# Optimization experiments

Hardware: AMD Instinct MI355X
Metric: run time of the kernel (lower is better)

## Reference

```python
import jax, jax.numpy as jnp
import numpy as np

B, C, Hf, Wf, HM, P = 64, 2048, 16, 16, 256, 10  # P = num_parts, NP = graph nodes
NP = P - 1
EPS = 1e-5  # BatchNorm eps

def bn_eval(x, g, b, rm, rv):
    return (x - rm) * jax.lax.rsqrt(rv + EPS) * g + b

def setup_inputs() -> dict:
    key = jax.random.key(0)
    ks = jax.random.split(key, 6)
    return {
        "x_global": jax.random.normal(ks[0], (B, C, Hf, Wf), jnp.float32),
        "x_gcn": jax.random.normal(ks[1], (B, C, Hf, Wf), jnp.float32),
        "mask": jax.random.randint(ks[2], (B, 1, HM, HM), 0, P, jnp.int32),
        "adj": jax.random.uniform(ks[3], (B, NP, NP), jnp.float32),
        "W1": jax.random.normal(ks[4], (C, C), jnp.float32) * 0.02,
        "b1": jnp.zeros((C,), jnp.float32),
        "g1": jnp.ones((NP * C,), jnp.float32), "be1": jnp.zeros((NP * C,), jnp.float32),
        "rm1": jnp.zeros((NP * C,), jnp.float32), "rv1": jnp.ones((NP * C,), jnp.float32),
        "W2": jax.random.normal(ks[5], (C, C), jnp.float32) * 0.02,
        "b2": jnp.zeros((C,), jnp.float32),
        "g2": jnp.ones((NP * C,), jnp.float32), "be2": jnp.zeros((NP * C,), jnp.float32),
        "rm2": jnp.zeros((NP * C,), jnp.float32), "rv2": jnp.ones((NP * C,), jnp.float32),
        "gb_g": jnp.ones((C,), jnp.float32), "gb_b": jnp.zeros((C,), jnp.float32),
        "gb_rm": jnp.zeros((C,), jnp.float32), "gb_rv": jnp.ones((C,), jnp.float32),
        "gn_g": jnp.ones((C,), jnp.float32), "gn_b": jnp.zeros((C,), jnp.float32),
        "gn_rm": jnp.zeros((C,), jnp.float32), "gn_rv": jnp.ones((C,), jnp.float32),
    }

def gc_layer(x, adj, Wt, bias, g, be, rm, rv):
    # GraphConvolution: matmul -> bmm(adj) -> bias -> BN over flattened (B, NP*C)
    s = jnp.einsum('bpc,cd->bpd', x, Wt)
    o = jnp.einsum('bpq,bqd->bpd', adj, s) + bias
    flat = o.reshape(o.shape[0], -1)
    return bn_eval(flat, g, be, rm, rv).reshape(o.shape)

def reference(x_global, x_gcn, mask, adj, W1, b1, g1, be1, rm1, rv1,
              W2, b2, g2, be2, rm2, rv2, gb_g, gb_b, gb_rm, gb_rv,
              gn_g, gn_b, gn_rm, gn_rv):
    # --- global branch: GAP + bottleneck BN (eval) ---
    feat_global = x_global.mean(axis=(2, 3))                      # (B, C)
    bnfeat_global = bn_eval(feat_global, gb_g, gb_b, gb_rm, gb_rv)

    # --- nearest-neighbor downsample of mask to feature-map size ---
    stride = HM // Hf
    mr = mask[:, 0, ::stride, ::stride]                           # (B, h, w)

    # one-hot part masks for classes 1..P-1: (B, h, w, NP)
    onehot = (mr[..., None] == jnp.arange(1, P)).astype(jnp.float32)
    counts = onehot.sum(axis=(1, 2))                              # (B, NP)

    # deterministic part dropout: drop the first present part per image
    drop = jnp.argmax(counts > 0, axis=1) + 1                     # (B,)
    keep = (mr != drop[:, None, None]).astype(jnp.float32)        # (B, h, w)
    x_self = x_gcn * keep[:, None, :, :]

    # segment mean pooling per part: (B, NP, C)
    denom = (counts + 1e-8)[..., None]
    mask_feat = jnp.einsum('bchw,bhwp->bpc', x_gcn, onehot) / denom
    self_feat = jnp.einsum('bchw,bhwp->bpc', x_self, onehot) / denom

    def gcn(x):
        x1 = jax.nn.relu(gc_layer(x, adj, W1, b1, g1, be1, rm1, rv1))
        x2 = jax.nn.relu(gc_layer(x1, adj, W2, b2, g2, be2, rm2, rv2))
        return x2.mean(axis=1), x2.reshape(x2.shape[0], -1)

    feat_gcn, feat_gcn_cat = gcn(mask_feat)
    feat_self, feat_self_cat = gcn(self_feat)
    bnfeat_gcn = bn_eval(feat_gcn, gn_g, gn_b, gn_rm, gn_rv)
    bnfeat_self = bn_eval(feat_self, gn_g, gn_b, gn_rm, gn_rv)

    # concatenate eval-mode outputs into one array: (B, 3*C + 2*NP*C)
    return jnp.concatenate([bnfeat_global, bnfeat_gcn, bnfeat_self,
                            feat_gcn_cat, feat_self_cat], axis=1)
```

## Files before the change

### kernel.cpp

```cpp
#include <hip/hip_runtime.h>
#include <cstdint>
#include <cstddef>

#define EPSV 1e-5f

typedef __bf16 bf16x8 __attribute__((ext_vector_type(8)));
typedef float f32x4 __attribute__((ext_vector_type(4)));

__device__ __forceinline__ unsigned short f2bf(float f) {
  unsigned int u = __float_as_uint(f);
  u += 0x7FFFu + ((u >> 16) & 1u);
  return (unsigned short)(u >> 16);
}

__device__ __forceinline__ void async_copy16(const void* src, void* dst_lds) {
  __builtin_amdgcn_global_load_lds(
      (const __attribute__((address_space(1))) void*)src,
      (__attribute__((address_space(3))) void*)dst_lds, 16, 0, 0);
}

__global__ __launch_bounds__(256) void prep(
    const float* __restrict__ W1, const float* __restrict__ W2,
    unsigned short* __restrict__ Wt1, unsigned short* __restrict__ Wt2,
    const float* __restrict__ xg, const float* __restrict__ gb_g,
    const float* __restrict__ gb_b, const float* __restrict__ gb_rm,
    const float* __restrict__ gb_rv, float* __restrict__ out,
    const int* __restrict__ mask, int* __restrict__ partid,
    float* __restrict__ invden, int* __restrict__ dropm1) {
  int blk = blockIdx.x;
  if (blk < 8192) {
    int z = blk >> 12;
    int rem = blk & 4095;
    int by = rem >> 6, bx = rem & 63;
    const float* W = z ? W2 : W1;
    unsigned short* Wt = z ? Wt2 : Wt1;
    __shared__ float tile[32][33];
    int tx = threadIdx.x & 31;
    int ty = threadIdx.x >> 5;
    int k0 = by * 32, n0 = bx * 32;
#pragma unroll
    for (int i = 0; i < 32; i += 8)
      tile[ty + i][tx] = W[(size_t)(k0 + ty + i) * 2048 + n0 + tx];
    __syncthreads();
#pragma unroll
    for (int i = 0; i < 32; i += 8)
      Wt[(size_t)(n0 + ty + i) * 2048 + k0 + tx] = f2bf(tile[tx][ty + i]);
  } else if (blk < 40960) {
    int gw = (blk - 8192) * 4 + (threadIdx.x >> 6);
    int lane = threadIdx.x & 63;
    float4 v = ((const float4*)(xg + (size_t)gw * 256))[lane];
    float s = v.x + v.y + v.z + v.w;
#pragma unroll
    for (int o = 32; o > 0; o >>= 1) s += __shfl_xor(s, o, 64);
    if (lane == 0) {
      int b = gw >> 11, c = gw & 2047;
      float m = s * (1.f / 256.f);
      out[(size_t)b * 43008 + c] =
          (m - gb_rm[c]) / sqrtf(gb_rv[c] + EPSV) * gb_g[c] + gb_b[c];
    }
  } else {
    int b = blk - 40960;
    int t = threadIdx.x;
    int h = t >> 4, w = t & 15;
    int m = mask[(size_t)b * 65536 + h * 4096 + w * 16];
    partid[b * 256 + t] = m;
    __shared__ int cnt[10];
    if (t < 10) cnt[t] = 0;
    __syncthreads();
    atomicAdd(&cnt[m], 1);
    __syncthreads();
    if (t == 0) {
      int dp = 0;
      for (int p = 8; p >= 0; p--)
        if (cnt[p + 1] > 0) dp = p;
      dropm1[b] = dp;
    }
    if (t < 9) invden[b * 9 + t] = 1.f / ((float)cnt[t + 1] + 1e-8f);
  }
}

__global__ __launch_bounds__(256) void kpool_mfma(
    const float* __restrict__ x, const int* __restrict__ partid,
    const float* __restrict__ invden, const int* __restrict__ dropm1,
    unsigned short* __restrict__ Abuf) {
  __shared__ unsigned short As[64 * 264];
  __shared__ unsigned short Bs[16 * 264];
  __shared__ int pid[256];
  const int t = threadIdx.x;
  const int b = blockIdx.y;
  const int c0 = blockIdx.x * 64;

  pid[t] = partid[b * 256 + t];

  const float4* xgp = (const float4*)(x + ((size_t)(b * 2048 + c0)) * 256);
#pragma unroll
  for (int it = 0; it < 16; it++) {
    int idx = t + it * 256;
    float4 v = xgp[idx];
    int row = idx >> 6, sc = (idx & 63) * 4;
    ushort4 h;
    h.x = f2bf(v.x); h.y = f2bf(v.y); h.z = f2bf(v.z); h.w = f2bf(v.w);
    *(ushort4*)&As[row * 264 + sc] = h;
  }
  __syncthreads();
  {
    int p = t >> 4, s0 = (t & 15) * 16;
#pragma unroll
    for (int j = 0; j < 16; j++)
      Bs[p * 264 + s0 + j] =
          (pid[s0 + j] == p + 1) ? (unsigned short)0x3F80 : (unsigned short)0;
  }
  __syncthreads();

  const int wave = t >> 6;
  const int l16 = t & 15;
  const int quad = (t & 63) >> 4;
  f32x4 acc = (f32x4){0.f, 0.f, 0.f, 0.f};
#pragma unroll
  for (int ks = 0; ks < 8; ks++) {
    bf16x8 a = *(const bf16x8*)&As[(wave * 16 + l16) * 264 + ks * 32 + quad * 8];
    bf16x8 bf = *(const bf16x8*)&Bs[l16 * 264 + ks * 32 + quad * 8];
    acc = __builtin_amdgcn_mfma_f32_16x16x32_bf16(a, bf, acc, 0, 0, 0);
  }

  if (l16 < 9) {
    int p = l16;
    float inv = invden[b * 9 + p];
    int dm1 = dropm1[b];
    int cbase = c0 + wave * 16 + quad * 4;
    ushort4 hm;
    hm.x = f2bf(acc[0] * inv);
    hm.y = f2bf(acc[1] * inv);
    hm.z = f2bf(acc[2] * inv);
    hm.w = f2bf(acc[3] * inv);
    ushort4 hs = (p == dm1) ? (ushort4){0, 0, 0, 0} : hm;
    *(ushort4*)&Abuf[(size_t)(b * 9 + p) * 2048 + cbase] = hm;
    *(ushort4*)&Abuf[(size_t)((64 + b) * 9 + p) * 2048 + cbase] = hs;
  }
}

#define GK 2048
#define SPART (1152 * 2048)
__global__ __launch_bounds__(256) void gemm_db(
    const unsigned short* __restrict__ A, const unsigned short* __restrict__ Bt,
    float* __restrict__ S) {
  __shared__ unsigned short As[2][128 * 64];
  __shared__ unsigned short Bs[2][128 * 64];
  const int tid = threadIdx.x;
  const int lane = tid & 63;
  const int wave = tid >> 6;
  const int wm = (wave >> 1) << 6;
  const int wn = (wave & 1) << 6;
  const int quad = lane >> 4;
  const int l16 = lane & 15;
  const int by = blockIdx.y;
  const int bx = blockIdx.x;
  const int kz = blockIdx.z;

  const unsigned short* Ag = A + (size_t)by * 128 * GK;
  const unsigned short* Bg = Bt + (size_t)bx * 128 * GK;
  S += (size_t)kz * SPART;

  f32x4 acc[4][4];
#pragma unroll
  for (int i = 0; i < 4; i++)
#pragma unroll
    for (int j = 0; j < 4; j++) acc[i][j] = (f32x4){0.f, 0.f, 0.f, 0.f};

  int srow[4], scol[4];
#pragma unroll
  for (int s = 0; s < 4; s++) {
    int idx = tid + s * 256;
    srow[s] = idx >> 3;
    scol[s] = ((idx & 7) ^ (srow[s] & 7)) * 8;
  }

  const int kbeg = kz * 512;

#define STAGE(buf, kk)                                                        \
  do {                                                                        \
    _Pragma("unroll") for (int s = 0; s < 4; s++) {                           \
      int idx = tid + s * 256;                                                \
      async_copy16(Ag + (size_t)srow[s] * GK + (kk) + scol[s],                \
                   &As[buf][idx * 8]);                                        \
    }                                                                         \
    _Pragma("unroll") for (int s = 0; s < 4; s++) {                           \
      int idx = tid + s * 256;                                                \
      async_copy16(Bg + (size_t)srow[s] * GK + (kk) + scol[s],                \
                   &Bs[buf][idx * 8]);                                        \
    }                                                                         \
  } while (0)

  STAGE(0, kbeg);
  asm volatile("s_waitcnt vmcnt(0)" ::: "memory");
  __syncthreads();

  for (int it = 0; it < 8; it++) {
    const int cur = it & 1;
    if (it < 7) STAGE(cur ^ 1, kbeg + (it + 1) * 64);

#pragma unroll
    for (int ks = 0; ks < 2; ks++) {
      bf16x8 af[4], bfr[4];
#pragma unroll
      for (int i = 0; i < 4; i++) {
        int row = wm + i * 16 + l16;
        int slot = row * 8 + ((ks * 4 + quad) ^ (row & 7));
        af[i] = *(const bf16x8*)&As[cur][slot * 8];
      }
#pragma unroll
      for (int j = 0; j < 4; j++) {
        int row = wn + j * 16 + l16;
        int slot = row * 8 + ((ks * 4 + quad) ^ (row & 7));
        bfr[j] = *(const bf16x8*)&Bs[cur][slot * 8];
      }
#pragma unroll
      for (int i = 0; i < 4; i++)
#pragma unroll
        for (int j = 0; j < 4; j++)
          acc[i][j] = __builtin_amdgcn_mfma_f32_16x16x32_bf16(
              af[i], bfr[j], acc[i][j], 0, 0, 0);
    }

    if (it < 7) {
      asm volatile("s_waitcnt vmcnt(0)" ::: "memory");
      __syncthreads();
    }
  }

#pragma unroll
  for (int i = 0; i < 4; i++)
#pragma unroll
    for (int j = 0; j < 4; j++)
#pragma unroll
      for (int r = 0; r < 4; r++) {
        int m = by * 128 + wm + i * 16 + quad * 4 + r;
        int n = bx * 128 + wn + j * 16 + l16;
        S[(size_t)m * 2048 + n] = acc[i][j][r];
      }
}

__global__ __launch_bounds__(256) void epi_mid(
    const float* __restrict__ S, const float* __restrict__ adj,
    const float* __restrict__ bias, const float* __restrict__ g,
    const float* __restrict__ be, const float* __restrict__ rm,
    const float* __restrict__ rv, unsigned short* __restrict__ Aout) {
  int idx = blockIdx.x * 256 + threadIdx.x;
  int d = idx & 2047;
  int bb = idx >> 11;
  int b = bb & 63;
  float s[9];
#pragma unroll
  for (int q = 0; q < 9; q++) {
    size_t off = (size_t)(bb * 9 + q) * 2048 + d;
    s[q] = S[off] + S[off + SPART] + S[off + 2 * SPART] + S[off + 3 * SPART];
  }
#pragma unroll
  for (int p = 0; p < 9; p++) {
    float o = bias[d];
#pragma unroll
    for (int q = 0; q < 9; q++) o += adj[b * 81 + p * 9 + q] * s[q];
    int f = p * 2048 + d;
    float v = (o - rm[f]) / sqrtf(rv[f] + EPSV) * g[f] + be[f];
    v = fmaxf(v, 0.f);
    Aout[(size_t)(bb * 9 + p) * 2048 + d] = f2bf(v);
  }
}

__global__ __launch_bounds__(256) void epi_final(
    const float* __restrict__ S, const float* __restrict__ adj,
    const float* __restrict__ bias, const float* __restrict__ g,
    const float* __restrict__ be, const float* __restrict__ rm,
    const float* __restrict__ rv, const float* __restrict__ gn_g,
    const float* __restrict__ gn_b, const float* __restrict__ gn_rm,
    const float* __restrict__ gn_rv, float* __restrict__ out) {
  int idx = blockIdx.x * 256 + threadIdx.x;
  int d = idx & 2047;
  int bb = idx >> 11;
  int b = bb & 63;
  bool selfb = bb >= 64;
  float s[9];
#pragma unroll
  for (int q = 0; q < 9; q++) {
    size_t off = (size_t)(bb * 9 + q) * 2048 + d;
    s[q] = S[off] + S[off + SPART] + S[off + 2 * SPART] + S[off + 3 * SPART];
  }
  float* orow = out + (size_t)b * 43008;
  size_t catbase = selfb ? 24576 : 6144;
  float mean = 0.f;
#pragma unroll
  for (int p = 0; p < 9; p++) {
    float o = bias[d];
#pragma unroll
    for (int q = 0; q < 9; q++) o += adj[b * 81 + p * 9 + q] * s[q];
    int f = p * 2048 + d;
    float v = (o - rm[f]) / sqrtf(rv[f] + EPSV) * g[f] + be[f];
    v = fmaxf(v, 0.f);
    mean += v;
    orow[catbase + f] = v;
  }
  mean *= (1.f / 9.f);
  orow[(selfb ? 4096 : 2048) + d] =
      (mean - gn_rm[d]) / sqrtf(gn_rv[d] + EPSV) * gn_g[d] + gn_b[d];
}

extern "C" void kernel_launch(void* const* d_in, const int* in_sizes, int n_in,
                              void* d_out, int out_size, void* d_ws,
                              size_t ws_size, hipStream_t stream) {
  const float* x_global = (const float*)d_in[0];
  const float* x_gcn = (const float*)d_in[1];
  const int* mask = (const int*)d_in[2];
  const float* adj = (const float*)d_in[3];
  const float* W1 = (const float*)d_in[4];
  const float* b1 = (const float*)d_in[5];
  const float* g1 = (const float*)d_in[6];
  const float* be1 = (const float*)d_in[7];
  const float* rm1 = (const float*)d_in[8];
  const float* rv1 = (const float*)d_in[9];
  const float* W2 = (const float*)d_in[10];
  const float* b2 = (const float*)d_in[11];
  const float* g2 = (const float*)d_in[12];
  const float* be2 = (const float*)d_in[13];
  const float* rm2 = (const float*)d_in[14];
  const float* rv2 = (const float*)d_in[15];
  const float* gb_g = (const float*)d_in[16];
  const float* gb_b = (const float*)d_in[17];
  const float* gb_rm = (const float*)d_in[18];
  const float* gb_rv = (const float*)d_in[19];
  const float* gn_g = (const float*)d_in[20];
  const float* gn_b = (const float*)d_in[21];
  const float* gn_rm = (const float*)d_in[22];
  const float* gn_rv = (const float*)d_in[23];
  float* out = (float*)d_out;

  char* ws = (char*)d_ws;
  int* partid = (int*)(ws);
  float* invden = (float*)(ws + 65536);
  int* dropm1 = (int*)(ws + 67840);
  unsigned short* Abuf = (unsigned short*)(ws + 131072);
  unsigned short* Wt1 = (unsigned short*)(ws + 4849664);
  unsigned short* Wt2 = (unsigned short*)(ws + 13238272);
  float* S = (float*)(ws + 21626880);

  prep<<<41024, 256, 0, stream>>>(W1, W2, Wt1, Wt2, x_global, gb_g, gb_b,
                                  gb_rm, gb_rv, out, mask, partid, invden,
                                  dropm1);
  kpool_mfma<<<dim3(32, 64), 256, 0, stream>>>(x_gcn, partid, invden, dropm1,
                                               Abuf);
  gemm_db<<<dim3(16, 9, 4), 256, 0, stream>>>(Abuf, Wt1, S);
  epi_mid<<<1024, 256, 0, stream>>>(S, adj, b1, g1, be1, rm1, rv1, Abuf);
  gemm_db<<<dim3(16, 9, 4), 256, 0, stream>>>(Abuf, Wt2, S);
  epi_final<<<1024, 256, 0, stream>>>(S, adj, b2, g2, be2, rm2, rv2, gn_g,
                                      gn_b, gn_rm, gn_rv, out);
}
```

Baseline: 411.1 us.

## Apply adjacency before the weight GEMM and fuse BN epilogue into GEMM

Uses associativity, adj·(X·W) = (adj·X)·W, so the 9x9 adjacency mix is applied to the pooled features in kpool (with the dropped part handled by subtracting its contribution) and to the layer-1 activations in a small kadj2 kernel. This lets the GEMM epilogue apply bias, BatchNorm and ReLU directly. The split-K partial-sum buffer S and its fp32 write and reduction traffic are removed. The GEMM now runs the full K loop per block over 144 blocks instead of 576, which lowers parallelism on a large GPU. The adj-mixed intermediate is rounded to bf16 before the GEMM, and the final mean is computed by re-reading the output.

```diff
diff --git a/kernel.cpp b/kernel.cpp
--- a/kernel.cpp
+++ b/kernel.cpp
@@ -11,6 +11,10 @@
   unsigned int u = __float_as_uint(f);
   u += 0x7FFFu + ((u >> 16) & 1u);
   return (unsigned short)(u >> 16);
+}
+
+__device__ __forceinline__ float bf2f(unsigned short h) {
+  return __uint_as_float(((unsigned int)h) << 16);
 }
 
 __device__ __forceinline__ void async_copy16(const void* src, void* dst_lds) {
@@ -82,10 +86,11 @@
 __global__ __launch_bounds__(256) void kpool_mfma(
     const float* __restrict__ x, const int* __restrict__ partid,
     const float* __restrict__ invden, const int* __restrict__ dropm1,
-    unsigned short* __restrict__ Abuf) {
+    const float* __restrict__ adj, unsigned short* __restrict__ A1) {
   __shared__ unsigned short As[64 * 264];
   __shared__ unsigned short Bs[16 * 264];
   __shared__ int pid[256];
+  __shared__ float sbuf[4][4][16][4];
   const int t = threadIdx.x;
   const int b = blockIdx.y;
   const int c0 = blockIdx.x * 64;
@@ -123,27 +128,50 @@
     acc = __builtin_amdgcn_mfma_f32_16x16x32_bf16(a, bf, acc, 0, 0, 0);
   }
 
+  {
+    float inv = (l16 < 9) ? invden[b * 9 + l16] : 0.f;
+    sbuf[wave][quad][l16][0] = acc[0] * inv;
+    sbuf[wave][quad][l16][1] = acc[1] * inv;
+    sbuf[wave][quad][l16][2] = acc[2] * inv;
+    sbuf[wave][quad][l16][3] = acc[3] * inv;
+  }
+  __syncthreads();
+
   if (l16 < 9) {
     int p = l16;
-    float inv = invden[b * 9 + p];
     int dm1 = dropm1[b];
+    const float* ap = adj + b * 81 + p * 9;
+    float om[4] = {0.f, 0.f, 0.f, 0.f};
+#pragma unroll
+    for (int q = 0; q < 9; q++) {
+      float aq = ap[q];
+#pragma unroll
+      for (int r = 0; r < 4; r++) om[r] += aq * sbuf[wave][quad][q][r];
+    }
+    float ad = ap[dm1];
+    float os[4];
+#pragma unroll
+    for (int r = 0; r < 4; r++) os[r] = om[r] - ad * sbuf[wave][quad][dm1][r];
+
     int cbase = c0 + wave * 16 + quad * 4;
-    ushort4 hm;
-    hm.x = f2bf(acc[0] * inv);
-    hm.y = f2bf(acc[1] * inv);
-    hm.z = f2bf(acc[2] * inv);
-    hm.w = f2bf(acc[3] * inv);
-    ushort4 hs = (p == dm1) ? (ushort4){0, 0, 0, 0} : hm;
-    *(ushort4*)&Abuf[(size_t)(b * 9 + p) * 2048 + cbase] = hm;
-    *(ushort4*)&Abuf[(size_t)((64 + b) * 9 + p) * 2048 + cbase] = hs;
+    ushort4 hm, hs;
+    hm.x = f2bf(om[0]); hm.y = f2bf(om[1]);
+    hm.z = f2bf(om[2]); hm.w = f2bf(om[3]);
+    hs.x = f2bf(os[0]); hs.y = f2bf(os[1]);
+    hs.z = f2bf(os[2]); hs.w = f2bf(os[3]);
+    *(ushort4*)&A1[(size_t)(b * 9 + p) * 2048 + cbase] = hm;
+    *(ushort4*)&A1[(size_t)((64 + b) * 9 + p) * 2048 + cbase] = hs;
   }
 }
 
 #define GK 2048
-#define SPART (1152 * 2048)
-__global__ __launch_bounds__(256) void gemm_db(
+template <int LAYER>
+__global__ __launch_bounds__(256) void gemm_fused(
     const unsigned short* __restrict__ A, const unsigned short* __restrict__ Bt,
-    float* __restrict__ S) {
+    const float* __restrict__ bias, const float* __restrict__ g,
+    const float* __restrict__ be, const float* __restrict__ rm,
+    const float* __restrict__ rv, unsigned short* __restrict__ Aout,
+    float* __restrict__ out) {
   __shared__ unsigned short As[2][128 * 64];
   __shared__ unsigned short Bs[2][128 * 64];
   const int tid = threadIdx.x;
@@ -155,11 +183,9 @@
   const int l16 = lane & 15;
   const int by = blockIdx.y;
   const int bx = blockIdx.x;
-  const int kz = blockIdx.z;
 
   const unsigned short* Ag = A + (size_t)by * 128 * GK;
   const unsigned short* Bg = Bt + (size_t)bx * 128 * GK;
-  S += (size_t)kz * SPART;
 
   f32x4 acc[4][4];
 #pragma unroll
@@ -174,8 +200,6 @@
     srow[s] = idx >> 3;
     scol[s] = ((idx & 7) ^ (srow[s] & 7)) * 8;
   }
-
-  const int kbeg = kz * 512;
 
 #define STAGE(buf, kk)                                                        \
   do {                                                                        \
@@ -191,13 +215,13 @@
     }                                                                         \
   } while (0)
 
-  STAGE(0, kbeg);
+  STAGE(0, 0);
   asm volatile("s_waitcnt vmcnt(0)" ::: "memory");
   __syncthreads();
 
-  for (int it = 0; it < 8; it++) {
+  for (int it = 0; it < 32; it++) {
     const int cur = it & 1;
-    if (it < 7) STAGE(cur ^ 1, kbeg + (it + 1) * 64);
+    if (it < 31) STAGE(cur ^ 1, (it + 1) * 64);
 
 #pragma unroll
     for (int ks = 0; ks < 2; ks++) {
@@ -222,7 +246,7 @@
               af[i], bfr[j], acc[i][j], 0, 0, 0);
     }
 
-    if (it < 7) {
+    if (it < 31) {
       asm volatile("s_waitcnt vmcnt(0)" ::: "memory");
       __syncthreads();
     }
@@ -231,77 +255,64 @@
 #pragma unroll
   for (int i = 0; i < 4; i++)
 #pragma unroll
-    for (int j = 0; j < 4; j++)
-#pragma unroll
-      for (int r = 0; r < 4; r++) {
-        int m = by * 128 + wm + i * 16 + quad * 4 + r;
+    for (int r = 0; r < 4; r++) {
+      int m = by * 128 + wm + i * 16 + quad * 4 + r;
+      int grp = m / 9;
+      int p = m - grp * 9;
+#pragma unroll
+      for (int j = 0; j < 4; j++) {
         int n = bx * 128 + wn + j * 16 + l16;
-        S[(size_t)m * 2048 + n] = acc[i][j][r];
+        int f = p * 2048 + n;
+        float v = acc[i][j][r] + bias[n];
+        v = (v - rm[f]) / sqrtf(rv[f] + EPSV) * g[f] + be[f];
+        v = fmaxf(v, 0.f);
+        if (LAYER == 1) {
+          Aout[(size_t)m * 2048 + n] = f2bf(v);
+        } else {
+          int b = grp & 63;
+          size_t base = (size_t)b * 43008 + ((grp >> 6) ? 24576 : 6144);
+          out[base + f] = v;
+        }
       }
-}
-
-__global__ __launch_bounds__(256) void epi_mid(
-    const float* __restrict__ S, const float* __restrict__ adj,
-    const float* __restrict__ bias, const float* __restrict__ g,
-    const float* __restrict__ be, const float* __restrict__ rm,
-    const float* __restrict__ rv, unsigned short* __restrict__ Aout) {
-  int idx = blockIdx.x * 256 + threadIdx.x;
-  int d = idx & 2047;
-  int bb = idx >> 11;
+    }
+}
+
+__global__ __launch_bounds__(256) void kadj2(
+    const unsigned short* __restrict__ A2, const float* __restrict__ adj,
+    unsigned short* __restrict__ A2p) {
+  int t = blockIdx.x * 256 + threadIdx.x;
+  int d = t & 2047;
+  int bb = t >> 11;
   int b = bb & 63;
   float s[9];
 #pragma unroll
-  for (int q = 0; q < 9; q++) {
-    size_t off = (size_t)(bb * 9 + q) * 2048 + d;
-    s[q] = S[off] + S[off + SPART] + S[off + 2 * SPART] + S[off + 3 * SPART];
-  }
+  for (int q = 0; q < 9; q++) s[q] = bf2f(A2[(size_t)(bb * 9 + q) * 2048 + d]);
+  const float* ap = adj + b * 81;
 #pragma unroll
   for (int p = 0; p < 9; p++) {
-    float o = bias[d];
-#pragma unroll
-    for (int q = 0; q < 9; q++) o += adj[b * 81 + p * 9 + q] * s[q];
-    int f = p * 2048 + d;
-    float v = (o - rm[f]) / sqrtf(rv[f] + EPSV) * g[f] + be[f];
-    v = fmaxf(v, 0.f);
-    Aout[(size_t)(bb * 9 + p) * 2048 + d] = f2bf(v);
-  }
-}
-
-__global__ __launch_bounds__(256) void epi_final(
-    const float* __restrict__ S, const float* __restrict__ adj,
-    const float* __restrict__ bias, const float* __restrict__ g,
-    const float* __restrict__ be, const float* __restrict__ rm,
-    const float* __restrict__ rv, const float* __restrict__ gn_g,
-    const float* __restrict__ gn_b, const float* __restrict__ gn_rm,
-    const float* __restrict__ gn_rv, float* __restrict__ out) {
-  int idx = blockIdx.x * 256 + threadIdx.x;
-  int d = idx & 2047;
-  int bb = idx >> 11;
-  int b = bb & 63;
-  bool selfb = bb >= 64;
-  float s[9];
-#pragma unroll
-  for (int q = 0; q < 9; q++) {
-    size_t off = (size_t)(bb * 9 + q) * 2048 + d;
-    s[q] = S[off] + S[off + SPART] + S[off + 2 * SPART] + S[off + 3 * SPART];
-  }
-  float* orow = out + (size_t)b * 43008;
-  size_t catbase = selfb ? 24576 : 6144;
-  float mean = 0.f;
-#pragma unroll
-  for (int p = 0; p < 9; p++) {
-    float o = bias[d];
-#pragma unroll
-    for (int q = 0; q < 9; q++) o += adj[b * 81 + p * 9 + q] * s[q];
-    int f = p * 2048 + d;
-    float v = (o - rm[f]) / sqrtf(rv[f] + EPSV) * g[f] + be[f];
-    v = fmaxf(v, 0.f);
-    mean += v;
-    orow[catbase + f] = v;
-  }
-  mean *= (1.f / 9.f);
-  orow[(selfb ? 4096 : 2048) + d] =
-      (mean - gn_rm[d]) / sqrtf(gn_rv[d] + EPSV) * gn_g[d] + gn_b[d];
+    float o = 0.f;
+#pragma unroll
+    for (int q = 0; q < 9; q++) o += ap[p * 9 + q] * s[q];
+    A2p[(size_t)(bb * 9 + p) * 2048 + d] = f2bf(o);
+  }
+}
+
+__global__ __launch_bounds__(256) void kfinal(
+    const float* __restrict__ gn_g, const float* __restrict__ gn_b,
+    const float* __restrict__ gn_rm, const float* __restrict__ gn_rv,
+    float* __restrict__ out) {
+  int t = blockIdx.x * 256 + threadIdx.x;
+  int d = t & 2047;
+  int grp = t >> 11;
+  int b = grp & 63;
+  int br = grp >> 6;
+  const float* src = out + (size_t)b * 43008 + (br ? 24576 : 6144) + d;
+  float s = 0.f;
+#pragma unroll
+  for (int p = 0; p < 9; p++) s += src[p * 2048];
+  s *= (1.f / 9.f);
+  out[(size_t)b * 43008 + (br ? 4096 : 2048) + d] =
+      (s - gn_rm[d]) / sqrtf(gn_rv[d] + EPSV) * gn_g[d] + gn_b[d];
 }
 
 extern "C" void kernel_launch(void* const* d_in, const int* in_sizes, int n_in,
@@ -337,19 +348,21 @@
   int* partid = (int*)(ws);
   float* invden = (float*)(ws + 65536);
   int* dropm1 = (int*)(ws + 67840);
-  unsigned short* Abuf = (unsigned short*)(ws + 131072);
-  unsigned short* Wt1 = (unsigned short*)(ws + 4849664);
-  unsigned short* Wt2 = (unsigned short*)(ws + 13238272);
-  float* S = (float*)(ws + 21626880);
+  unsigned short* A1 = (unsigned short*)(ws + 131072);
+  unsigned short* A2 = (unsigned short*)(ws + 4849664);
+  unsigned short* A2p = (unsigned short*)(ws + 9568256);
+  unsigned short* Wt1 = (unsigned short*)(ws + 14286848);
+  unsigned short* Wt2 = (unsigned short*)(ws + 22675456);
 
   prep<<<41024, 256, 0, stream>>>(W1, W2, Wt1, Wt2, x_global, gb_g, gb_b,
                                   gb_rm, gb_rv, out, mask, partid, invden,
                                   dropm1);
   kpool_mfma<<<dim3(32, 64), 256, 0, stream>>>(x_gcn, partid, invden, dropm1,
-                                               Abuf);
-  gemm_db<<<dim3(16, 9, 4), 256, 0, stream>>>(Abuf, Wt1, S);
-  epi_mid<<<1024, 256, 0, stream>>>(S, adj, b1, g1, be1, rm1, rv1, Abuf);
-  gemm_db<<<dim3(16, 9, 4), 256, 0, stream>>>(Abuf, Wt2, S);
-  epi_final<<<1024, 256, 0, stream>>>(S, adj, b2, g2, be2, rm2, rv2, gn_g,
-                                      gn_b, gn_rm, gn_rv, out);
-}
+                                               adj, A1);
+  gemm_fused<1><<<dim3(16, 9), 256, 0, stream>>>(A1, Wt1, b1, g1, be1, rm1,
+                                                 rv1, A2, nullptr);
+  kadj2<<<1024, 256, 0, stream>>>(A2, adj, A2p);
+  gemm_fused<2><<<dim3(16, 9), 256, 0, stream>>>(A2p, Wt2, b2, g2, be2, rm2,
+                                                 rv2, nullptr, out);
+  kfinal<<<1024, 256, 0, stream>>>(gn_g, gn_b, gn_rm, gn_rv, out);
+}
```

Result: slower. 477.1 us (+16.1%).
